# Kernel optimization log

Measured on AMD Instinct MI355X. Metric: run time of the kernel, lower is better.

Reference implementation:

```python
import jax, jax.numpy as jnp
import numpy as np

NB_CLASSES = 256
EMBEDDING_SIZE = 50
TOTAL_CHARS = 8_000_000
NUM_WORDS = 1_600_000


def setup_inputs() -> dict:
    key = jax.random.key(0)
    k1, k2, k3 = jax.random.split(key, 3)
    char_ids = jax.random.randint(k1, (TOTAL_CHARS,), 0, NB_CLASSES, dtype=jnp.int64 if jax.config.jax_enable_x64 else jnp.int32)
    segment_ids = jnp.sort(jax.random.randint(k2, (TOTAL_CHARS,), 0, NUM_WORDS, dtype=char_ids.dtype))
    embedding_table = jax.random.normal(k3, (NB_CLASSES, EMBEDDING_SIZE), dtype=jnp.float32)
    return {
        "char_ids": char_ids,
        "segment_ids": segment_ids,
        "num_words": NUM_WORDS,
        "embedding_table": embedding_table,
    }


def reference(char_ids, segment_ids, num_words, embedding_table):
    # Fused ragged gather + segment-mean: equivalent to, for each word,
    # mean over its characters of embedding_table[char].
    char_emb = embedding_table[char_ids]                      # [total_chars, E]
    sums = jax.ops.segment_sum(char_emb, segment_ids, num_segments=num_words)  # [num_words, E]
    counts = jax.ops.segment_sum(
        jnp.ones((char_ids.shape[0],), dtype=embedding_table.dtype),
        segment_ids, num_segments=num_words)                  # [num_words]
    counts = jnp.maximum(counts, 1.0)                         # guard empty words
    return sums / counts[:, None]                             # [num_words, E]
```

## Files before the change

### kernel.cpp

```cpp
#include <hip/hip_runtime.h>


#define EMB 50
#define EMB2 25

__global__ __launch_bounds__(256) void seg_starts_kernel(
    const int* __restrict__ seg, int* __restrict__ starts, int n, int num_words) {
  int i = blockIdx.x * blockDim.x + threadIdx.x;
  if (i > n) return;
  int cur  = (i < n) ? seg[i]     : num_words;
  int prev = (i > 0) ? seg[i - 1] : -1;
  for (int w = prev + 1; w <= cur; ++w) starts[w] = i;
}

__global__ __launch_bounds__(256) void word_mean_kernel(
    const int* __restrict__ char_ids, const float* __restrict__ table,
    const int* __restrict__ starts, float* __restrict__ out, int num_words) {
  int w = blockIdx.x * blockDim.x + threadIdx.x;
  if (w >= num_words) return;
  int s = starts[w];
  int e = starts[w + 1];

  float ax[EMB2], ay[EMB2];
#pragma unroll
  for (int k = 0; k < EMB2; ++k) { ax[k] = 0.f; ay[k] = 0.f; }

  for (int i = s; i < e; ++i) {
    int c = char_ids[i];
    const float2* row = (const float2*)(table + c * EMB);
#pragma unroll
    for (int k = 0; k < EMB2; ++k) {
      float2 v = row[k];
      ax[k] += v.x;
      ay[k] += v.y;
    }
  }

  int cnt = e - s;
  float inv = (cnt > 0) ? (1.0f / (float)cnt) : 0.0f;
  float2* orow = (float2*)(out + (size_t)w * EMB);
#pragma unroll
  for (int k = 0; k < EMB2; ++k) {
    orow[k] = make_float2(ax[k] * inv, ay[k] * inv);
  }
}

__device__ __forceinline__ int lb(const int* __restrict__ seg, int n, int w) {
  int lo = 0, hi = n;
  while (lo < hi) {
    int mid = (lo + hi) >> 1;
    if (seg[mid] < w) lo = mid + 1; else hi = mid;
  }
  return lo;
}

__global__ __launch_bounds__(256) void word_mean_bs_kernel(
    const int* __restrict__ char_ids, const int* __restrict__ seg,
    const float* __restrict__ table, float* __restrict__ out, int n, int num_words) {
  int w = blockIdx.x * blockDim.x + threadIdx.x;
  if (w >= num_words) return;
  int s = lb(seg, n, w);
  int e = lb(seg, n, w + 1);

  float ax[EMB2], ay[EMB2];
#pragma unroll
  for (int k = 0; k < EMB2; ++k) { ax[k] = 0.f; ay[k] = 0.f; }

  for (int i = s; i < e; ++i) {
    int c = char_ids[i];
    const float2* row = (const float2*)(table + c * EMB);
#pragma unroll
    for (int k = 0; k < EMB2; ++k) {
      float2 v = row[k];
      ax[k] += v.x;
      ay[k] += v.y;
    }
  }

  int cnt = e - s;
  float inv = (cnt > 0) ? (1.0f / (float)cnt) : 0.0f;
  float2* orow = (float2*)(out + (size_t)w * EMB);
#pragma unroll
  for (int k = 0; k < EMB2; ++k) {
    orow[k] = make_float2(ax[k] * inv, ay[k] * inv);
  }
}

extern "C" void kernel_launch(void* const* d_in, const int* in_sizes, int n_in,
                              void* d_out, int out_size, void* d_ws, size_t ws_size,
                              hipStream_t stream) {
  const int*   char_ids = (const int*)d_in[0];
  const int*   seg      = (const int*)d_in[1];
  const float* table    = (const float*)d_in[3];
  float*       out      = (float*)d_out;

  const int n  = in_sizes[0];
  const int nw = out_size / EMB;

  if (ws_size >= (size_t)(nw + 1) * sizeof(int)) {
    int* starts = (int*)d_ws;
    seg_starts_kernel<<<(n + 256) / 256, 256, 0, stream>>>(seg, starts, n, nw);
    word_mean_kernel<<<(nw + 255) / 256, 256, 0, stream>>>(char_ids, table, starts, out, nw);
  } else {
    word_mean_bs_kernel<<<(nw + 255) / 256, 256, 0, stream>>>(char_ids, seg, table, out, n, nw);
  }
}
```

Baseline: 564.1 us.

## Stage embedding table in LDS and map threads to word-column pairs

Restructures the word-mean kernel so each 1024-thread block copies the 51KB embedding table into shared memory, then uses a grid-stride loop over (word, float2-column) pairs. Each thread accumulates one column pair, which gives coalesced output writes and drops the 50-register accumulator arrays per thread, raising occupancy. The segment-start kernel now handles four sorted ids per thread with int4 loads. The trade-offs are redundant reads of starts and char_ids (25 threads per word), a per-block table copy, and LDS bank conflicts on the random row gathers.

```diff
diff --git a/kernel.cpp b/kernel.cpp
--- a/kernel.cpp
+++ b/kernel.cpp
@@ -1,89 +1,85 @@
 #include <hip/hip_runtime.h>
 
 
+#define NB 256
 #define EMB 50
-#define EMB2 25
+#define PAIRS 25
+#define BLK 1024
 
-__global__ __launch_bounds__(256) void seg_starts_kernel(
-    const int* __restrict__ seg, int* __restrict__ starts, int n, int num_words) {
-  int i = blockIdx.x * blockDim.x + threadIdx.x;
-  if (i > n) return;
-  int cur  = (i < n) ? seg[i]     : num_words;
-  int prev = (i > 0) ? seg[i - 1] : -1;
-  for (int w = prev + 1; w <= cur; ++w) starts[w] = i;
+__global__ __launch_bounds__(256) void seg_starts4(
+    const int* __restrict__ seg, int* __restrict__ starts, int n, int nw) {
+  int base = (blockIdx.x * blockDim.x + threadIdx.x) * 4;
+  if (base >= n) return;
+  int lim = n - base; if (lim > 4) lim = 4;
+  int vals[4];
+  if (lim == 4) {
+    int4 v = *(const int4*)(seg + base);
+    vals[0] = v.x; vals[1] = v.y; vals[2] = v.z; vals[3] = v.w;
+  } else {
+    for (int u = 0; u < lim; ++u) vals[u] = seg[base + u];
+  }
+  int prev = (base > 0) ? seg[base - 1] : -1;
+  for (int u = 0; u < lim; ++u) {
+    int cur = vals[u];
+    for (int w = prev + 1; w <= cur; ++w) starts[w] = base + u;
+    prev = cur;
+  }
+  if (base + lim == n) {
+    for (int w = prev + 1; w <= nw; ++w) starts[w] = n;
+  }
 }
 
-__global__ __launch_bounds__(256) void word_mean_kernel(
+__global__ __launch_bounds__(BLK, 8) void word_mean_v2(
     const int* __restrict__ char_ids, const float* __restrict__ table,
-    const int* __restrict__ starts, float* __restrict__ out, int num_words) {
-  int w = blockIdx.x * blockDim.x + threadIdx.x;
-  if (w >= num_words) return;
-  int s = starts[w];
-  int e = starts[w + 1];
+    const int* __restrict__ starts, float2* __restrict__ out2, int num_words) {
+  __shared__ __align__(16) float tab[NB * EMB];
+  for (int idx = threadIdx.x; idx < NB * EMB / 4; idx += BLK)
+    ((float4*)tab)[idx] = ((const float4*)table)[idx];
+  __syncthreads();
 
-  float ax[EMB2], ay[EMB2];
-#pragma unroll
-  for (int k = 0; k < EMB2; ++k) { ax[k] = 0.f; ay[k] = 0.f; }
-
-  for (int i = s; i < e; ++i) {
-    int c = char_ids[i];
-    const float2* row = (const float2*)(table + c * EMB);
-#pragma unroll
-    for (int k = 0; k < EMB2; ++k) {
-      float2 v = row[k];
-      ax[k] += v.x;
-      ay[k] += v.y;
+  const int total  = num_words * PAIRS;
+  const int stride = gridDim.x * BLK;
+  for (int t = blockIdx.x * BLK + threadIdx.x; t < total; t += stride) {
+    int w  = t / PAIRS;
+    int k2 = (t - w * PAIRS) * 2;
+    int s = starts[w];
+    int e = starts[w + 1];
+    float sx = 0.f, sy = 0.f;
+    for (int i = s; i < e; ++i) {
+      int c = char_ids[i];
+      float2 v = *(const float2*)(tab + c * EMB + k2);
+      sx += v.x; sy += v.y;
     }
-  }
-
-  int cnt = e - s;
-  float inv = (cnt > 0) ? (1.0f / (float)cnt) : 0.0f;
-  float2* orow = (float2*)(out + (size_t)w * EMB);
-#pragma unroll
-  for (int k = 0; k < EMB2; ++k) {
-    orow[k] = make_float2(ax[k] * inv, ay[k] * inv);
+    int cnt = e - s;
+    float inv = (cnt > 0) ? (1.0f / (float)cnt) : 0.0f;
+    out2[t] = make_float2(sx * inv, sy * inv);
   }
 }
 
 __device__ __forceinline__ int lb(const int* __restrict__ seg, int n, int w) {
   int lo = 0, hi = n;
-  while (lo < hi) {
-    int mid = (lo + hi) >> 1;
-    if (seg[mid] < w) lo = mid + 1; else hi = mid;
-  }
+  while (lo < hi) { int m = (lo + hi) >> 1; if (seg[m] < w) lo = m + 1; else hi = m; }
   return lo;
 }
-
 __global__ __launch_bounds__(256) void word_mean_bs_kernel(
     const int* __restrict__ char_ids, const int* __restrict__ seg,
     const float* __restrict__ table, float* __restrict__ out, int n, int num_words) {
   int w = blockIdx.x * blockDim.x + threadIdx.x;
   if (w >= num_words) return;
-  int s = lb(seg, n, w);
-  int e = lb(seg, n, w + 1);
-
-  float ax[EMB2], ay[EMB2];
+  int s = lb(seg, n, w), e = lb(seg, n, w + 1);
+  float ax[PAIRS], ay[PAIRS];
 #pragma unroll
-  for (int k = 0; k < EMB2; ++k) { ax[k] = 0.f; ay[k] = 0.f; }
-
+  for (int k = 0; k < PAIRS; ++k) { ax[k] = 0.f; ay[k] = 0.f; }
   for (int i = s; i < e; ++i) {
-    int c = char_ids[i];
-    const float2* row = (const float2*)(table + c * EMB);
+    const float2* row = (const float2*)(table + char_ids[i] * EMB);
 #pragma unroll
-    for (int k = 0; k < EMB2; ++k) {
-      float2 v = row[k];
-      ax[k] += v.x;
-      ay[k] += v.y;
-    }
+    for (int k = 0; k < PAIRS; ++k) { float2 v = row[k]; ax[k] += v.x; ay[k] += v.y; }
   }
-
   int cnt = e - s;
   float inv = (cnt > 0) ? (1.0f / (float)cnt) : 0.0f;
   float2* orow = (float2*)(out + (size_t)w * EMB);
 #pragma unroll
-  for (int k = 0; k < EMB2; ++k) {
-    orow[k] = make_float2(ax[k] * inv, ay[k] * inv);
-  }
+  for (int k = 0; k < PAIRS; ++k) orow[k] = make_float2(ax[k] * inv, ay[k] * inv);
 }
 
 extern "C" void kernel_launch(void* const* d_in, const int* in_sizes, int n_in,
@@ -99,9 +95,12 @@
 
   if (ws_size >= (size_t)(nw + 1) * sizeof(int)) {
     int* starts = (int*)d_ws;
-    seg_starts_kernel<<<(n + 256) / 256, 256, 0, stream>>>(seg, starts, n, nw);
-    word_mean_kernel<<<(nw + 255) / 256, 256, 0, stream>>>(char_ids, table, starts, out, nw);
+    int nchunk = (n + 3) / 4;
+    seg_starts4<<<(nchunk + 255) / 256, 256, 0, stream>>>(seg, starts, n, nw);
+    word_mean_v2<<<512, BLK, 0, stream>>>(char_ids, table, starts,
+                                          (float2*)out, nw);
   } else {
-    word_mean_bs_kernel<<<(nw + 255) / 256, 256, 0, stream>>>(char_ids, seg, table, out, n, nw);
+    word_mean_bs_kernel<<<(nw + 255) / 256, 256, 0, stream>>>(
+        char_ids, seg, table, out, n, nw);
   }
 }
```

Result: faster. 546.9 us (-3.1%).
